# Kernel tuning notes

Measured on AMD Instinct MI355X. Metric: run time of the kernel, lower is better.

## Reference

```python
import jax, jax.numpy as jnp
import numpy as np

K_MAX = 64      # config.k_max
N_HASH = 8      # LSH hash bits per table


def setup_inputs() -> dict:
    key = jax.random.key(0)
    kq, kk, kw = jax.random.split(key, 3)
    B, L, D = 4, 2048, 64
    query = jax.random.normal(kq, (B, L, D), dtype=jnp.float32)
    key_t = jax.random.normal(kk, (B, L, D), dtype=jnp.float32)
    W = jax.random.normal(kw, (D, N_HASH), dtype=jnp.float32)  # LSH projection
    return {"query": query, "key": key_t, "W": W, "head_idx": 0}


def _hash_code(x, W):
    # binary_quantize then LSH hash: sign bits of random projection, packed to one int code
    x_bin = jnp.where(x > 0, 1.0, 0.0)                      # [B,L,D]
    bits = (jnp.einsum('bld,dh->blh', x_bin, W) > 0)        # [B,L,H] bool
    weights = (2 ** jnp.arange(N_HASH, dtype=jnp.int32))    # pack bits -> bucket id
    return jnp.sum(bits.astype(jnp.int32) * weights, axis=-1)  # [B,L] int32


def reference(query, key, W, head_idx):
    B, L, _ = query.shape
    q_code = _hash_code(query, W)   # [B,L]
    k_code = _hash_code(key, W)     # [B,L]
    # hash-equality match matrix [B, Lq, Lk] (== .all(dim=2) on hash bits)
    matches = q_code[:, :, None] == k_code[:, None, :]
    idx = jnp.arange(L, dtype=jnp.int32)
    # non-matches get sentinel L so the k_max smallest indices are the first matches
    cand_keys = jnp.where(matches, idx[None, None, :], L)   # [B,L,L]
    neg_top, _ = jax.lax.top_k(-cand_keys, K_MAX)           # k_max smallest indices
    cand = -neg_top                                          # ascending first-match order
    return jnp.where(cand == L, -1, cand).astype(jnp.int64)  # [B,L,k_max], -1 padded
```

## Files before the change

### kernel.cpp

```cpp
#include <hip/hip_runtime.h>

#define D 64
#define H 8
#define LSEQ 2048
#define KMAX 64
#define NCODES 256

__global__ void __launch_bounds__(256)
code_kernel(const float* __restrict__ query,
            const float* __restrict__ key,
            const float* __restrict__ W,
            int* __restrict__ q_code,
            int* __restrict__ k_code,
            int n_pos) {
    __shared__ float Ws[D * H];
    for (int i = threadIdx.x; i < D * H; i += blockDim.x) Ws[i] = W[i];
    __syncthreads();

    int t = blockIdx.x * blockDim.x + threadIdx.x;
    if (t >= 2 * n_pos) return;

    const float* xp = (t < n_pos) ? (query + (size_t)t * D)
                                  : (key + (size_t)(t - n_pos) * D);
    float4 s0 = {0.f, 0.f, 0.f, 0.f};
    float4 s1 = {0.f, 0.f, 0.f, 0.f};

    for (int d4 = 0; d4 < D / 4; ++d4) {
        float4 xv = ((const float4*)xp)[d4];
        const float* x4 = (const float*)&xv;
#pragma unroll
        for (int k = 0; k < 4; ++k) {
            if (x4[k] > 0.0f) {
                int d = d4 * 4 + k;
                float4 w0 = *(const float4*)&Ws[d * H + 0];
                float4 w1 = *(const float4*)&Ws[d * H + 4];
                s0.x += w0.x; s0.y += w0.y; s0.z += w0.z; s0.w += w0.w;
                s1.x += w1.x; s1.y += w1.y; s1.z += w1.z; s1.w += w1.w;
            }
        }
    }
    int c = 0;
    c |= (s0.x > 0.0f) ? 1   : 0;
    c |= (s0.y > 0.0f) ? 2   : 0;
    c |= (s0.z > 0.0f) ? 4   : 0;
    c |= (s0.w > 0.0f) ? 8   : 0;
    c |= (s1.x > 0.0f) ? 16  : 0;
    c |= (s1.y > 0.0f) ? 32  : 0;
    c |= (s1.z > 0.0f) ? 64  : 0;
    c |= (s1.w > 0.0f) ? 128 : 0;

    if (t < n_pos) q_code[t] = c;
    else           k_code[t - n_pos] = c;
}

__global__ void __launch_bounds__(256)
scan_emit_kernel(const int* __restrict__ q_code,
                 const int* __restrict__ k_code,
                 int* __restrict__ out) {
    __shared__ int rows[4][KMAX];
    int wave = threadIdx.x >> 6;
    int lane = threadIdx.x & 63;
    int q = blockIdx.x * 4 + wave;
    int b = q >> 11;

    int c = q_code[q];
    const int* kc = k_code + (size_t)b * LSEQ;
    int* row = rows[wave];
    row[lane] = -1;

    unsigned long long lt_mask = (lane == 63) ? 0x7FFFFFFFFFFFFFFFull
                                              : ((1ull << lane) - 1ull);
    int base = 0;
    for (int i = 0; i < LSEQ / 64; ++i) {
        int idx = i * 64 + lane;
        int ci = kc[idx];
        unsigned long long mask = __ballot(ci == c);
        if (ci == c) {
            int rank = base + __popcll(mask & lt_mask);
            if (rank < KMAX) row[rank] = idx;
        }
        base += __popcll(mask);
        if (base >= KMAX) break;
    }
    out[(size_t)q * KMAX + lane] = row[lane];
}

extern "C" void kernel_launch(void* const* d_in, const int* in_sizes, int n_in,
                              void* d_out, int out_size, void* d_ws, size_t ws_size,
                              hipStream_t stream) {
    const float* query = (const float*)d_in[0];
    const float* key   = (const float*)d_in[1];
    const float* W     = (const float*)d_in[2];

    int n_pos = in_sizes[0] / D;
    (void)ws_size;

    int* q_code = (int*)d_ws;
    int* k_code = q_code + n_pos;

    {
        int total = 2 * n_pos;
        code_kernel<<<(total + 255) / 256, 256, 0, stream>>>(query, key, W,
                                                             q_code, k_code, n_pos);
    }
    {
        scan_emit_kernel<<<n_pos / 4, 256, 0, stream>>>(q_code, k_code,
                                                        (int*)d_out);
    }
}
```

Baseline: 78.52 us.

## Pack key codes as bytes in lane-interleaved layout and prefetch full row

Key hash codes are now stored as single bytes, permuted so that each lane's 32-bit word holds four codes for consecutive 64-key chunks. The scan kernel preloads all eight words per lane up front and unrolls the ballot loop over them, which cuts key-code traffic fourfold and removes the serialized per-chunk load latency. In exchange the early exit once KMAX matches are found is dropped, so every wave always runs all 32 ballots. The code kernel's block size also drops from 256 to 64 threads.

After: 73.87 us. -5.9%, faster.

```diff
diff --git a/kernel.cpp b/kernel.cpp
--- a/kernel.cpp
+++ b/kernel.cpp
@@ -6,12 +6,12 @@
 #define KMAX 64
 #define NCODES 256
 
-__global__ void __launch_bounds__(256)
+__global__ void __launch_bounds__(64)
 code_kernel(const float* __restrict__ query,
             const float* __restrict__ key,
             const float* __restrict__ W,
             int* __restrict__ q_code,
-            int* __restrict__ k_code,
+            unsigned char* __restrict__ kperm,
             int n_pos) {
     __shared__ float Ws[D * H];
     for (int i = threadIdx.x; i < D * H; i += blockDim.x) Ws[i] = W[i];
@@ -49,13 +49,22 @@
     c |= (s1.z > 0.0f) ? 64  : 0;
     c |= (s1.w > 0.0f) ? 128 : 0;
 
-    if (t < n_pos) q_code[t] = c;
-    else           k_code[t - n_pos] = c;
+    if (t < n_pos) {
+        q_code[t] = c;
+    } else {
+        int kk = t - n_pos;
+        int b    = kk >> 11;
+        int l    = kk & (LSEQ - 1);
+        int lane = l & 63;
+        int j    = (l >> 6) & 3;
+        int i4   = l >> 8;
+        kperm[(b << 11) + (i4 << 8) + (lane << 2) + j] = (unsigned char)c;
+    }
 }
 
 __global__ void __launch_bounds__(256)
 scan_emit_kernel(const int* __restrict__ q_code,
-                 const int* __restrict__ k_code,
+                 const unsigned int* __restrict__ kperm,
                  int* __restrict__ out) {
     __shared__ int rows[4][KMAX];
     int wave = threadIdx.x >> 6;
@@ -64,23 +73,30 @@
     int b = q >> 11;
 
     int c = q_code[q];
-    const int* kc = k_code + (size_t)b * LSEQ;
+    const unsigned int* kp = kperm + (size_t)b * (LSEQ / 4) + lane;
     int* row = rows[wave];
     row[lane] = -1;
+
+    unsigned int v[LSEQ / 256];
+#pragma unroll
+    for (int i = 0; i < LSEQ / 256; ++i) v[i] = kp[i * 64];
 
     unsigned long long lt_mask = (lane == 63) ? 0x7FFFFFFFFFFFFFFFull
                                               : ((1ull << lane) - 1ull);
     int base = 0;
-    for (int i = 0; i < LSEQ / 64; ++i) {
-        int idx = i * 64 + lane;
-        int ci = kc[idx];
-        unsigned long long mask = __ballot(ci == c);
-        if (ci == c) {
-            int rank = base + __popcll(mask & lt_mask);
-            if (rank < KMAX) row[rank] = idx;
+#pragma unroll
+    for (int i = 0; i < LSEQ / 256; ++i) {
+        unsigned int w = v[i];
+#pragma unroll
+        for (int j = 0; j < 4; ++j) {
+            int ci = (int)((w >> (8 * j)) & 0xFFu);
+            unsigned long long mask = __ballot(ci == c);
+            if (ci == c) {
+                int rank = base + __popcll(mask & lt_mask);
+                if (rank < KMAX) row[rank] = i * 256 + j * 64 + lane;
+            }
+            base += __popcll(mask);
         }
-        base += __popcll(mask);
-        if (base >= KMAX) break;
     }
     out[(size_t)q * KMAX + lane] = row[lane];
 }
@@ -96,15 +112,16 @@
     (void)ws_size;
 
     int* q_code = (int*)d_ws;
-    int* k_code = q_code + n_pos;
+    unsigned char* kperm = (unsigned char*)(q_code + n_pos);
 
     {
         int total = 2 * n_pos;
-        code_kernel<<<(total + 255) / 256, 256, 0, stream>>>(query, key, W,
-                                                             q_code, k_code, n_pos);
+        code_kernel<<<(total + 63) / 64, 64, 0, stream>>>(query, key, W,
+                                                          q_code, kperm, n_pos);
     }
     {
-        scan_emit_kernel<<<n_pos / 4, 256, 0, stream>>>(q_code, k_code,
+        scan_emit_kernel<<<n_pos / 4, 256, 0, stream>>>(q_code,
+                                                        (const unsigned int*)kperm,
                                                         (int*)d_out);
     }
 }
```
